# Kernel optimization log

Measured on AMD Instinct MI355X. Metric: run time of the kernel, lower is better.

## Reference

```python
import jax, jax.numpy as jnp
import numpy as np

B, S, D, H, HID = 4, 2048, 1024, 16, 4096
DK = D // H
EPS = 1e-6


def layernorm(x, alpha, bias):
    # Matches the custom LayerNorm: std with Bessel correction (torch default),
    # and eps added to std (not variance).
    mean = jnp.mean(x, axis=-1, keepdims=True)
    std = jnp.std(x, axis=-1, ddof=1, keepdims=True)
    return alpha * (x - mean) / (std + EPS) + bias


def setup_inputs() -> dict:
    key = jax.random.key(0)
    ks = jax.random.split(key, 10)
    s = 0.02
    return {
        "x": jax.random.normal(ks[0], (B, S, D), dtype=jnp.float32),
        "wq": jax.random.normal(ks[1], (D, D), dtype=jnp.float32) * s,
        "wk": jax.random.normal(ks[2], (D, D), dtype=jnp.float32) * s,
        "wv": jax.random.normal(ks[3], (D, D), dtype=jnp.float32) * s,
        "wo": jax.random.normal(ks[4], (D, D), dtype=jnp.float32) * s,
        "w1": jax.random.normal(ks[5], (D, HID), dtype=jnp.float32) * s,
        "b1": jnp.zeros((HID,), dtype=jnp.float32),
        "w2": jax.random.normal(ks[6], (HID, D), dtype=jnp.float32) * s,
        "b2": jnp.zeros((D,), dtype=jnp.float32),
        "ln1_a": jnp.ones((D,), dtype=jnp.float32),
        "ln1_b": jnp.zeros((D,), dtype=jnp.float32),
        "ln2_a": jnp.ones((D,), dtype=jnp.float32),
        "ln2_b": jnp.zeros((D,), dtype=jnp.float32),
    }


def reference(x, wq, wk, wv, wo, w1, b1, w2, b2, ln1_a, ln1_b, ln2_a, ln2_b):
    # --- residual 1: pre-norm self-attention ---
    h = layernorm(x, ln1_a, ln1_b)
    q = (h @ wq).reshape(B, S, H, DK)
    k = (h @ wk).reshape(B, S, H, DK)
    v = (h @ wv).reshape(B, S, H, DK)
    scores = jnp.einsum("bqhd,bkhd->bhqk", q, k) / jnp.sqrt(jnp.float32(DK))
    # Faithful replication of the original mask: tril on a (1, max_len) matrix
    # keeps only key position 0; all other key positions get -1e9.
    key_keep = (jnp.arange(S) == 0)  # [S]
    scores = jnp.where(key_keep[None, None, None, :], scores, jnp.float32(-1e9))
    attn = jax.nn.softmax(scores, axis=-1)  # [B,H,S,S]
    ctx = jnp.einsum("bhqk,bkhd->bqhd", attn, v).reshape(B, S, D)
    x = x + ctx @ wo
    # --- residual 2: pre-norm FFN ---
    h2 = layernorm(x, ln2_a, ln2_b)
    ff = jax.nn.gelu(h2 @ w1 + b1, approximate=False) @ w2 + b2
    return x + ff
```

## Files before the change

### kernel.cpp

```cpp
#include <hip/hip_runtime.h>
#include <cstdint>

#define D_MODEL 1024
#define HIDDEN  4096
#define BATCH   4
#define SEQ     2048
#define NROWS   (BATCH*SEQ)

typedef __attribute__((ext_vector_type(4))) int i32x4;

#define ACT_AMAX 4.0f
#define ACT_S    (ACT_AMAX / 127.0f)
#define ACT_INV  (127.0f / ACT_AMAX)

#define GLDS16(g, l) __builtin_amdgcn_global_load_lds(                        \
    (const __attribute__((address_space(1))) unsigned int*)(g),               \
    (__attribute__((address_space(3))) unsigned int*)(l), 16, 0, 0)

__device__ __forceinline__ float block_sum(float v, float* s4) {
  #pragma unroll
  for (int off = 32; off > 0; off >>= 1) v += __shfl_down(v, off);
  int lane = threadIdx.x & 63, wid = threadIdx.x >> 6;
  __syncthreads();
  if (lane == 0) s4[wid] = v;
  __syncthreads();
  return s4[0] + s4[1] + s4[2] + s4[3];
}

__device__ __forceinline__ float block_max(float v, float* s4) {
  #pragma unroll
  for (int off = 32; off > 0; off >>= 1) v = fmaxf(v, __shfl_down(v, off));
  int lane = threadIdx.x & 63, wid = threadIdx.x >> 6;
  __syncthreads();
  if (lane == 0) s4[wid] = v;
  __syncthreads();
  return fmaxf(fmaxf(s4[0], s4[1]), fmaxf(s4[2], s4[3]));
}

__device__ __forceinline__ signed char qclamp(float v) {
  float r = rintf(v);
  r = fminf(127.f, fmaxf(-127.f, r));
  return (signed char)(int)r;
}

#define KCHUNKS 32
#define KCH     (D_MODEL / KCHUNKS)


__device__ __forceinline__ void absmax_cols_body(
    const float* __restrict__ in, int R, int C, unsigned* __restrict__ u,
    int bx, int by) {
  int c  = bx * 256 + threadIdx.x;
  int r0 = by * 64;
  float m = 0.f;
  #pragma unroll 4
  for (int r = 0; r < 64; ++r)
    m = fmaxf(m, fabsf(in[(size_t)(r0 + r) * C + c]));
  atomicMax(&u[c], __float_as_uint(m));
}

__device__ __forceinline__ void transpose_quant_body(
    const float* __restrict__ in, signed char* __restrict__ out,
    int R, int C, const unsigned* __restrict__ u,
    float (*tile)[33], int bx, int by) {
  int c0 = bx * 32, r0 = by * 32;
  int tx = threadIdx.x & 31, ty = threadIdx.x >> 5;
  #pragma unroll
  for (int i = ty; i < 32; i += 8)
    tile[i][tx] = in[(size_t)(r0 + i) * C + c0 + tx];
  __syncthreads();
  #pragma unroll
  for (int i = ty; i < 32; i += 8) {
    float f = __uint_as_float(u[c0 + i]);
    float inv = f > 0.f ? 127.f / f : 0.f;
    out[(size_t)(c0 + i) * R + r0 + tx] = qclamp(tile[tx][i] * inv);
  }
}

__device__ __forceinline__ void ln_matvec_body(
    const float* __restrict__ x, const float* __restrict__ ln_a,
    const float* __restrict__ ln_b, const float* __restrict__ W,
    float* __restrict__ vout, float* s4, float (*hs)[KCH], int bx, int by) {
  int n  = bx * 256 + threadIdx.x;
  int k0 = by * KCH;
  int t  = threadIdx.x;
  float4 g4 = ((const float4*)ln_a)[t];
  float4 b4 = ((const float4*)ln_b)[t];
  #pragma unroll
  for (int b = 0; b < 4; ++b) {
    const float* xr = x + (size_t)b * SEQ * D_MODEL;
    float4 v = ((const float4*)xr)[t];
    float sum = v.x + v.y + v.z + v.w;
    float mean = block_sum(sum, s4) * (1.f / 1024.f);
    float cx = v.x - mean, cy = v.y - mean, cz = v.z - mean, cw = v.w - mean;
    float sq = cx * cx + cy * cy + cz * cz + cw * cw;
    float var = block_sum(sq, s4) * (1.f / 1023.f);
    float inv = 1.f / (sqrtf(var) + 1e-6f);
    if (t >= (k0 >> 2) && t < ((k0 + KCH) >> 2)) {
      int lc = 4 * t - k0;
      hs[b][lc + 0] = g4.x * cx * inv + b4.x;
      hs[b][lc + 1] = g4.y * cy * inv + b4.y;
      hs[b][lc + 2] = g4.z * cz * inv + b4.z;
      hs[b][lc + 3] = g4.w * cw * inv + b4.w;
    }
  }
  __syncthreads();
  float a0 = 0, a1 = 0, a2 = 0, a3 = 0;
  #pragma unroll
  for (int k = 0; k < KCH; ++k) {
    float w = W[(size_t)(k0 + k) * D_MODEL + n];
    a0 = fmaf(hs[0][k], w, a0);
    a1 = fmaf(hs[1][k], w, a1);
    a2 = fmaf(hs[2][k], w, a2);
    a3 = fmaf(hs[3][k], w, a3);
  }
  atomicAdd(&vout[0 * D_MODEL + n], a0);
  atomicAdd(&vout[1 * D_MODEL + n], a1);
  atomicAdd(&vout[2 * D_MODEL + n], a2);
  atomicAdd(&vout[3 * D_MODEL + n], a3);
}

__device__ __forceinline__ void matvec_body(
    const float* __restrict__ vin, const float* __restrict__ W,
    float* __restrict__ vout, float (*hs)[KCH], int bx, int by) {
  int n  = bx * 256 + threadIdx.x;
  int k0 = by * KCH;
  if (threadIdx.x < 4 * KCH)
    hs[threadIdx.x / KCH][threadIdx.x % KCH] =
        vin[(threadIdx.x / KCH) * D_MODEL + k0 + (threadIdx.x % KCH)];
  __syncthreads();
  float a0 = 0, a1 = 0, a2 = 0, a3 = 0;
  #pragma unroll
  for (int k = 0; k < KCH; ++k) {
    float w = W[(size_t)(k0 + k) * D_MODEL + n];
    a0 = fmaf(hs[0][k], w, a0);
    a1 = fmaf(hs[1][k], w, a1);
    a2 = fmaf(hs[2][k], w, a2);
    a3 = fmaf(hs[3][k], w, a3);
  }
  atomicAdd(&vout[0 * D_MODEL + n], a0);
  atomicAdd(&vout[1 * D_MODEL + n], a1);
  atomicAdd(&vout[2 * D_MODEL + n], a2);
  atomicAdd(&vout[3 * D_MODEL + n], a3);
}

__global__ __launch_bounds__(256) void pre1(
    const float* __restrict__ w1, const float* __restrict__ w2,
    unsigned* __restrict__ u1, unsigned* __restrict__ u2,
    const float* __restrict__ x, const float* __restrict__ ln1a,
    const float* __restrict__ ln1b, const float* __restrict__ wv,
    float* __restrict__ v0) {
  __shared__ float s4[4];
  __shared__ float hs[4][KCH];
  int id = blockIdx.x;
  if (id < 256) {
    absmax_cols_body(w1, D_MODEL, HIDDEN, u1, id & 15, id >> 4);
  } else if (id < 512) {
    int r = id - 256;
    absmax_cols_body(w2, HIDDEN, D_MODEL, u2, r & 3, r >> 2);
  } else {
    int r = id - 512;
    ln_matvec_body(x, ln1a, ln1b, wv, v0, s4, hs, r & 3, r >> 2);
  }
}

__global__ __launch_bounds__(256) void pre2(
    const float* __restrict__ w1, const float* __restrict__ w2,
    const unsigned* __restrict__ u1, const unsigned* __restrict__ u2,
    signed char* __restrict__ w1t, signed char* __restrict__ w2t,
    const float* __restrict__ v0, const float* __restrict__ wo,
    float* __restrict__ delta) {
  __shared__ float tile[32][33];
  __shared__ float hs[4][KCH];
  int id = blockIdx.x;
  if (id < 4096) {
    transpose_quant_body(w1, w1t, D_MODEL, HIDDEN, u1, tile, id & 127, id >> 7);
  } else if (id < 8192) {
    int r = id - 4096;
    transpose_quant_body(w2, w2t, HIDDEN, D_MODEL, u2, tile, r & 31, r >> 5);
  } else {
    int r = id - 8192;
    matvec_body(v0, wo, delta, hs, r & 3, r >> 2);
  }
}

__global__ __launch_bounds__(256) void fused_res_ln_q(
    const float* __restrict__ x, const float* __restrict__ delta,
    const float* __restrict__ g, const float* __restrict__ be,
    float* __restrict__ x1_out, signed char* __restrict__ h2,
    float* __restrict__ hscale) {
  __shared__ float s4[4];
  int row = blockIdx.x;
  int b = row >> 11;
  int t = threadIdx.x;
  float4 v  = ((const float4*)(x + (size_t)row * D_MODEL))[t];
  float4 d4 = ((const float4*)(delta + (size_t)b * D_MODEL))[t];
  v.x += d4.x; v.y += d4.y; v.z += d4.z; v.w += d4.w;
  float sum = v.x + v.y + v.z + v.w;
  float mean = block_sum(sum, s4) * (1.f / 1024.f);
  float cx = v.x - mean, cy = v.y - mean, cz = v.z - mean, cw = v.w - mean;
  float sq = cx * cx + cy * cy + cz * cz + cw * cw;
  float var = block_sum(sq, s4) * (1.f / 1023.f);
  float inv = 1.f / (sqrtf(var) + 1e-6f);
  ((float4*)(x1_out + (size_t)row * D_MODEL))[t] = v;
  float4 g4 = ((const float4*)g)[t];
  float4 b4 = ((const float4*)be)[t];
  float h0v = g4.x * cx * inv + b4.x;
  float h1v = g4.y * cy * inv + b4.y;
  float h2v = g4.z * cz * inv + b4.z;
  float h3v = g4.w * cw * inv + b4.w;
  float am = fmaxf(fmaxf(fabsf(h0v), fabsf(h1v)), fmaxf(fabsf(h2v), fabsf(h3v)));
  float amax = block_max(am, s4);
  float qs = amax > 0.f ? 127.f / amax : 0.f;
  unsigned q = ((unsigned)(unsigned char)(int)qclamp(h0v * qs)) |
               ((unsigned)(unsigned char)(int)qclamp(h1v * qs) << 8) |
               ((unsigned)(unsigned char)(int)qclamp(h2v * qs) << 16) |
               ((unsigned)(unsigned char)(int)qclamp(h3v * qs) << 24);
  ((unsigned*)(h2 + (size_t)row * D_MODEL))[t] = q;
  if (t == 0) hscale[row] = amax * (1.f / 127.f);
}

template <int EPI>
__global__ __launch_bounds__(256, 3) void gemm_i8(
    const signed char* __restrict__ A, const signed char* __restrict__ Bt,
    const float* __restrict__ rowS, float rowConst,
    const unsigned* __restrict__ colU, const float* __restrict__ bias,
    signed char* __restrict__ Cq, float* __restrict__ Cf, int M, int N, int K) {
  __shared__ signed char LA[128][128];
  __shared__ signed char LB[128][128];

  int GN  = N / 128;
  int nwg = (M / 128) * GN;
  int id  = blockIdx.x;
  int sw  = (id & 7) * (nwg >> 3) + (id >> 3);
  int by  = sw / GN, bx = sw % GN;
  int m0  = by * 128, n0 = bx * 128;
  int NT  = K / 128;

  int t = threadIdx.x;
  int wid = t >> 6, lane = t & 63;
  int wm = wid >> 1, wn = wid & 1;
  int lr = lane & 15, kg = lane >> 4;
  int swz = (lr & 7) << 4;

  int rS = t >> 3;
  int cS = ((t & 7) ^ (rS & 7)) * 16;
  const signed char* Ag = A  + (size_t)(m0 + rS) * K + cS;
  const signed char* Bg = Bt + (size_t)(n0 + rS) * K + cS;
  int ldsOff = wid * 1024;

#define STG_T(T) do {                                                          \
    size_t ko_ = (size_t)(T) * 128;                                            \
    GLDS16(Ag + ko_,                  &LA[0][0] + ldsOff);                     \
    GLDS16(Ag + ko_ + (size_t)32 * K, &LA[0][0] + ldsOff + 4096);              \
    GLDS16(Ag + ko_ + (size_t)64 * K, &LA[0][0] + ldsOff + 8192);              \
    GLDS16(Ag + ko_ + (size_t)96 * K, &LA[0][0] + ldsOff + 12288);             \
    GLDS16(Bg + ko_,                  &LB[0][0] + ldsOff);                     \
    GLDS16(Bg + ko_ + (size_t)32 * K, &LB[0][0] + ldsOff + 4096);              \
    GLDS16(Bg + ko_ + (size_t)64 * K, &LB[0][0] + ldsOff + 8192);              \
    GLDS16(Bg + ko_ + (size_t)96 * K, &LB[0][0] + ldsOff + 12288);             \
  } while (0)

#define RD_AB() do {                                                           \
    _Pragma("unroll") for (int mi = 0; mi < 4; ++mi)                           \
    _Pragma("unroll") for (int kk = 0; kk < 2; ++kk)                           \
      a[mi][kk] = *(const i32x4*)                                              \
          &LA[wm * 64 + mi * 16 + lr][(kk * 64 + kg * 16) ^ swz];              \
    _Pragma("unroll") for (int ni = 0; ni < 4; ++ni)                           \
    _Pragma("unroll") for (int kk = 0; kk < 2; ++kk)                           \
      b[ni][kk] = *(const i32x4*)                                              \
          &LB[wn * 64 + ni * 16 + lr][(kk * 64 + kg * 16) ^ swz];              \
  } while (0)

#define MM_ALL() do {                                                          \
    _Pragma("unroll") for (int mi = 0; mi < 4; ++mi)                           \
    _Pragma("unroll") for (int ni = 0; ni < 4; ++ni)                           \
    _Pragma("unroll") for (int kk = 0; kk < 2; ++kk)                           \
      acc[mi][ni] = __builtin_amdgcn_mfma_i32_16x16x64_i8(                     \
          a[mi][kk], b[ni][kk], acc[mi][ni], 0, 0, 0);                         \
  } while (0)

  i32x4 acc[4][4] = {};
  i32x4 a[4][2];
  i32x4 b[4][2];

  for (int tt = 0; tt < NT; ++tt) {
    STG_T(tt);
    asm volatile("s_waitcnt vmcnt(0)" ::: "memory");
    __builtin_amdgcn_s_barrier();
    RD_AB();
    MM_ALL();
    __builtin_amdgcn_s_barrier();
  }

  int orow = m0 + wm * 64;
  int ocol = n0 + wn * 64;
  #pragma unroll
  for (int mf = 0; mf < 4; ++mf) {
    #pragma unroll
    for (int nf = 0; nf < 4; ++nf) {
      int col = ocol + nf * 16 + lr;
      float cs = __uint_as_float(colU[col]) * (1.f / 127.f);
      float bz = bias[col];
      #pragma unroll
      for (int j = 0; j < 4; ++j) {
        int row = orow + mf * 16 + kg * 4 + j;
        float rs = (EPI == 0) ? rowS[row] : rowConst;
        float val = (float)acc[mf][nf][j] * rs * cs + bz;
        if (EPI == 0) {
          float u = val * (0.7978845608f + 0.0356774081f * val * val);
          float e = __expf(2.f * u);
          float th = 1.f - 2.f / (e + 1.f);
          val = 0.5f * val * (1.f + th);
          Cq[(size_t)row * N + col] = qclamp(val * ACT_INV);
        } else {
          size_t idx = (size_t)row * N + col;
          Cf[idx] = Cf[idx] + val;
        }
      }
    }
  }
#undef STG_T
#undef RD_AB
#undef MM_ALL
}

__global__ __launch_bounds__(256, 3) void gemm2_sk2(
    const signed char* __restrict__ A, const signed char* __restrict__ Bt,
    const unsigned* __restrict__ colU, const float* __restrict__ bias,
    float* __restrict__ Cf) {
  constexpr int M = NROWS, N = D_MODEL, K = HIDDEN;
  constexpr int GN = N / 128;
  constexpr int PS = (M / 128) * GN;
  constexpr int NT = (K / 2) / 128;

  __shared__ signed char LA[128][128];
  __shared__ signed char LB[128][128];

  int id = blockIdx.x;
  int sw = (id & 7) * 128 + (id >> 3);
  int ks = sw >> 9;
  int rem = sw & (PS - 1);
  int by = rem >> 3, bx = rem & (GN - 1);
  int m0 = by * 128, n0 = bx * 128;
  int k0s = ks * (K / 2);

  int t = threadIdx.x;
  int wid = t >> 6, lane = t & 63;
  int wm = wid >> 1, wn = wid & 1;
  int lr = lane & 15, kg = lane >> 4;
  int swz = (lr & 7) << 4;

  int rS = t >> 3;
  int cS = ((t & 7) ^ (rS & 7)) * 16;
  const signed char* Ag = A  + (size_t)(m0 + rS) * K + k0s + cS;
  const signed char* Bg = Bt + (size_t)(n0 + rS) * K + k0s + cS;
  int ldsOff = wid * 1024;

#define STG_T(T) do {                                                          \
    size_t ko_ = (size_t)(T) * 128;                                            \
    GLDS16(Ag + ko_,                  &LA[0][0] + ldsOff);                     \
    GLDS16(Ag + ko_ + (size_t)32 * K, &LA[0][0] + ldsOff + 4096);              \
    GLDS16(Ag + ko_ + (size_t)64 * K, &LA[0][0] + ldsOff + 8192);              \
    GLDS16(Ag + ko_ + (size_t)96 * K, &LA[0][0] + ldsOff + 12288);             \
    GLDS16(Bg + ko_,                  &LB[0][0] + ldsOff);                     \
    GLDS16(Bg + ko_ + (size_t)32 * K, &LB[0][0] + ldsOff + 4096);              \
    GLDS16(Bg + ko_ + (size_t)64 * K, &LB[0][0] + ldsOff + 8192);              \
    GLDS16(Bg + ko_ + (size_t)96 * K, &LB[0][0] + ldsOff + 12288);             \
  } while (0)

#define RD_AB() do {                                                           \
    _Pragma("unroll") for (int mi = 0; mi < 4; ++mi)                           \
    _Pragma("unroll") for (int kk = 0; kk < 2; ++kk)                           \
      a[mi][kk] = *(const i32x4*)                                              \
          &LA[wm * 64 + mi * 16 + lr][(kk * 64 + kg * 16) ^ swz];              \
    _Pragma("unroll") for (int ni = 0; ni < 4; ++ni)                           \
    _Pragma("unroll") for (int kk = 0; kk < 2; ++kk)                           \
      b[ni][kk] = *(const i32x4*)                                              \
          &LB[wn * 64 + ni * 16 + lr][(kk * 64 + kg * 16) ^ swz];              \
  } while (0)

#define MM_ALL() do {                                                          \
    _Pragma("unroll") for (int mi = 0; mi < 4; ++mi)                           \
    _Pragma("unroll") for (int ni = 0; ni < 4; ++ni)                           \
    _Pragma("unroll") for (int kk = 0; kk < 2; ++kk)                           \
      acc[mi][ni] = __builtin_amdgcn_mfma_i32_16x16x64_i8(                     \
          a[mi][kk], b[ni][kk], acc[mi][ni], 0, 0, 0);                         \
  } while (0)

  i32x4 acc[4][4] = {};
  i32x4 a[4][2];
  i32x4 b[4][2];

  for (int tt = 0; tt < NT; ++tt) {
    STG_T(tt);
    asm volatile("s_waitcnt vmcnt(0)" ::: "memory");
    __builtin_amdgcn_s_barrier();
    RD_AB();
    MM_ALL();
    __builtin_amdgcn_s_barrier();
  }

  int orow = m0 + wm * 64;
  int ocol = n0 + wn * 64;
  #pragma unroll
  for (int mf = 0; mf < 4; ++mf) {
    #pragma unroll
    for (int nf = 0; nf < 4; ++nf) {
      int col = ocol + nf * 16 + lr;
      float cs = __uint_as_float(colU[col]) * (1.f / 127.f);
      float bz = (ks == 0) ? bias[col] : 0.f;
      #pragma unroll
      for (int j = 0; j < 4; ++j) {
        int row = orow + mf * 16 + kg * 4 + j;
        float val = (float)acc[mf][nf][j] * ACT_S * cs + bz;
        atomicAdd(&Cf[(size_t)row * N + col], val);
      }
    }
  }
#undef STG_T
#undef RD_AB
#undef MM_ALL
}

extern "C" void kernel_launch(void* const* d_in, const int* in_sizes, int n_in,
                              void* d_out, int out_size, void* d_ws, size_t ws_size,
                              hipStream_t stream) {
  const float* x    = (const float*)d_in[0];
  const float* wv   = (const float*)d_in[3];
  const float* wo   = (const float*)d_in[4];
  const float* w1   = (const float*)d_in[5];
  const float* b1   = (const float*)d_in[6];
  const float* w2   = (const float*)d_in[7];
  const float* b2   = (const float*)d_in[8];
  const float* ln1a = (const float*)d_in[9];
  const float* ln1b = (const float*)d_in[10];
  const float* ln2a = (const float*)d_in[11];
  const float* ln2b = (const float*)d_in[12];
  float* out = (float*)d_out;

  char* ws = (char*)d_ws;
  signed char* w1t = (signed char*)(ws);
  signed char* w2t = (signed char*)(ws + (4ull  << 20));
  signed char* h2  = (signed char*)(ws + (8ull  << 20));
  signed char* act = (signed char*)(ws + (16ull << 20));
  char* sc = ws + (48ull << 20);
  unsigned* u1    = (unsigned*)(sc);
  unsigned* u2    = (unsigned*)(sc + 16384);
  float*    v0    = (float*)(sc + 20480);
  float*    delta = (float*)(sc + 36864);
  float*    hsc   = (float*)(sc + 53248);

  hipMemsetAsync(sc, 0, 53248, stream);

  pre1<<<640, 256, 0, stream>>>(w1, w2, u1, u2, x, ln1a, ln1b, wv, v0);

  pre2<<<8320, 256, 0, stream>>>(w1, w2, u1, u2, w1t, w2t, v0, wo, delta);

  fused_res_ln_q<<<NROWS, 256, 0, stream>>>(x, delta, ln2a, ln2b, out, h2, hsc);

  gemm_i8<0><<<(NROWS / 128) * (HIDDEN / 128), 256, 0, stream>>>(
      h2, w1t, hsc, 0.f, u1, b1, act, nullptr, NROWS, HIDDEN, D_MODEL);

  gemm2_sk2<<<1024, 256, 0, stream>>>(act, w2t, u2, b2, out);
}
```

Before: 197.0 us.

## Replace split-K atomic GEMM2 with K=256 tile kernel and XCD-aware block mapping

The second FFN GEMM drops its 2-way split-K with atomicAdd epilogue and becomes a templated kernel that stages 256-wide K slices per iteration (double the LDS per block, occupancy hint lowered to 2) and does a plain read-add-write into the output. Both GEMMs also replace the strided block swizzle with a mapping that gives each XCD a contiguous 2D region of output tiles, aiming for better L2 reuse per die. The intent is to remove atomic traffic and halve barrier and loop overhead per K. The cost is 512 blocks instead of 1024 for GEMM2, less parallelism and lower occupancy.

```diff
diff --git a/kernel.cpp b/kernel.cpp
--- a/kernel.cpp
+++ b/kernel.cpp
@@ -221,7 +221,7 @@
 }
 
 template <int EPI>
-__global__ __launch_bounds__(256, 3) void gemm_i8(
+__global__ __launch_bounds__(256, 3) void gemm_k128(
     const signed char* __restrict__ A, const signed char* __restrict__ Bt,
     const float* __restrict__ rowS, float rowConst,
     const unsigned* __restrict__ colU, const float* __restrict__ bias,
@@ -230,10 +230,14 @@
   __shared__ signed char LB[128][128];
 
   int GN  = N / 128;
-  int nwg = (M / 128) * GN;
+  int CX  = (GN >= 16) ? 16 : (GN >> 1);
   int id  = blockIdx.x;
-  int sw  = (id & 7) * (nwg >> 3) + (id >> 3);
-  int by  = sw / GN, bx = sw % GN;
+  int xcd = id & 7;
+  int r   = id >> 3;
+  int cby = xcd >> 1, cbx = xcd & 1;
+  int lby = r / CX,   lbx = r % CX;
+  int by  = cby * 16 + lby;
+  int bx  = cbx * CX + lbx;
   int m0  = by * 128, n0 = bx * 128;
   int NT  = K / 128;
 
@@ -325,25 +329,26 @@
 #undef MM_ALL
 }
 
-__global__ __launch_bounds__(256, 3) void gemm2_sk2(
+template <int EPI>
+__global__ __launch_bounds__(256, 2) void gemm_k256(
     const signed char* __restrict__ A, const signed char* __restrict__ Bt,
+    const float* __restrict__ rowS, float rowConst,
     const unsigned* __restrict__ colU, const float* __restrict__ bias,
-    float* __restrict__ Cf) {
-  constexpr int M = NROWS, N = D_MODEL, K = HIDDEN;
-  constexpr int GN = N / 128;
-  constexpr int PS = (M / 128) * GN;
-  constexpr int NT = (K / 2) / 128;
-
-  __shared__ signed char LA[128][128];
-  __shared__ signed char LB[128][128];
-
-  int id = blockIdx.x;
-  int sw = (id & 7) * 128 + (id >> 3);
-  int ks = sw >> 9;
-  int rem = sw & (PS - 1);
-  int by = rem >> 3, bx = rem & (GN - 1);
-  int m0 = by * 128, n0 = bx * 128;
-  int k0s = ks * (K / 2);
+    signed char* __restrict__ Cq, float* __restrict__ Cf, int M, int N, int K) {
+  __shared__ signed char LA[128][256];
+  __shared__ signed char LB[128][256];
+
+  int GN  = N / 128;
+  int CX  = (GN >= 16) ? 16 : (GN >> 1);
+  int id  = blockIdx.x;
+  int xcd = id & 7;
+  int r   = id >> 3;
+  int cby = xcd >> 1, cbx = xcd & 1;
+  int lby = r / CX,   lbx = r % CX;
+  int by  = cby * 16 + lby;
+  int bx  = cbx * CX + lbx;
+  int m0  = by * 128, n0 = bx * 128;
+  int NT  = K / 256;
 
   int t = threadIdx.x;
   int wid = t >> 6, lane = t & 63;
@@ -351,31 +356,29 @@
   int lr = lane & 15, kg = lane >> 4;
   int swz = (lr & 7) << 4;
 
-  int rS = t >> 3;
-  int cS = ((t & 7) ^ (rS & 7)) * 16;
-  const signed char* Ag = A  + (size_t)(m0 + rS) * K + k0s + cS;
-  const signed char* Bg = Bt + (size_t)(n0 + rS) * K + k0s + cS;
+  int rS = t >> 4;
+  int cS = ((t & 15) ^ (rS & 7)) * 16;
+  const signed char* Ag = A  + (size_t)(m0 + rS) * K + cS;
+  const signed char* Bg = Bt + (size_t)(n0 + rS) * K + cS;
   int ldsOff = wid * 1024;
 
 #define STG_T(T) do {                                                          \
-    size_t ko_ = (size_t)(T) * 128;                                            \
-    GLDS16(Ag + ko_,                  &LA[0][0] + ldsOff);                     \
-    GLDS16(Ag + ko_ + (size_t)32 * K, &LA[0][0] + ldsOff + 4096);              \
-    GLDS16(Ag + ko_ + (size_t)64 * K, &LA[0][0] + ldsOff + 8192);              \
-    GLDS16(Ag + ko_ + (size_t)96 * K, &LA[0][0] + ldsOff + 12288);             \
-    GLDS16(Bg + ko_,                  &LB[0][0] + ldsOff);                     \
-    GLDS16(Bg + ko_ + (size_t)32 * K, &LB[0][0] + ldsOff + 4096);              \
-    GLDS16(Bg + ko_ + (size_t)64 * K, &LB[0][0] + ldsOff + 8192);              \
-    GLDS16(Bg + ko_ + (size_t)96 * K, &LB[0][0] + ldsOff + 12288);             \
+    size_t ko_ = (size_t)(T) * 256;                                            \
+    _Pragma("unroll") for (int j = 0; j < 8; ++j)                              \
+      GLDS16(Ag + ko_ + (size_t)(16 * j) * K,                                  \
+             &LA[0][0] + ldsOff + j * 4096);                                   \
+    _Pragma("unroll") for (int j = 0; j < 8; ++j)                              \
+      GLDS16(Bg + ko_ + (size_t)(16 * j) * K,                                  \
+             &LB[0][0] + ldsOff + j * 4096);                                   \
   } while (0)
 
 #define RD_AB() do {                                                           \
     _Pragma("unroll") for (int mi = 0; mi < 4; ++mi)                           \
-    _Pragma("unroll") for (int kk = 0; kk < 2; ++kk)                           \
+    _Pragma("unroll") for (int kk = 0; kk < 4; ++kk)                           \
       a[mi][kk] = *(const i32x4*)                                              \
           &LA[wm * 64 + mi * 16 + lr][(kk * 64 + kg * 16) ^ swz];              \
     _Pragma("unroll") for (int ni = 0; ni < 4; ++ni)                           \
-    _Pragma("unroll") for (int kk = 0; kk < 2; ++kk)                           \
+    _Pragma("unroll") for (int kk = 0; kk < 4; ++kk)                           \
       b[ni][kk] = *(const i32x4*)                                              \
           &LB[wn * 64 + ni * 16 + lr][(kk * 64 + kg * 16) ^ swz];              \
   } while (0)
@@ -383,14 +386,14 @@
 #define MM_ALL() do {                                                          \
     _Pragma("unroll") for (int mi = 0; mi < 4; ++mi)                           \
     _Pragma("unroll") for (int ni = 0; ni < 4; ++ni)                           \
-    _Pragma("unroll") for (int kk = 0; kk < 2; ++kk)                           \
+    _Pragma("unroll") for (int kk = 0; kk < 4; ++kk)                           \
       acc[mi][ni] = __builtin_amdgcn_mfma_i32_16x16x64_i8(                     \
           a[mi][kk], b[ni][kk], acc[mi][ni], 0, 0, 0);                         \
   } while (0)
 
   i32x4 acc[4][4] = {};
-  i32x4 a[4][2];
-  i32x4 b[4][2];
+  i32x4 a[4][4];
+  i32x4 b[4][4];
 
   for (int tt = 0; tt < NT; ++tt) {
     STG_T(tt);
@@ -409,12 +412,22 @@
     for (int nf = 0; nf < 4; ++nf) {
       int col = ocol + nf * 16 + lr;
       float cs = __uint_as_float(colU[col]) * (1.f / 127.f);
-      float bz = (ks == 0) ? bias[col] : 0.f;
+      float bz = bias[col];
       #pragma unroll
       for (int j = 0; j < 4; ++j) {
         int row = orow + mf * 16 + kg * 4 + j;
-        float val = (float)acc[mf][nf][j] * ACT_S * cs + bz;
-        atomicAdd(&Cf[(size_t)row * N + col], val);
+        float rs = (EPI == 0) ? rowS[row] : rowConst;
+        float val = (float)acc[mf][nf][j] * rs * cs + bz;
+        if (EPI == 0) {
+          float u = val * (0.7978845608f + 0.0356774081f * val * val);
+          float e = __expf(2.f * u);
+          float th = 1.f - 2.f / (e + 1.f);
+          val = 0.5f * val * (1.f + th);
+          Cq[(size_t)row * N + col] = qclamp(val * ACT_INV);
+        } else {
+          size_t idx = (size_t)row * N + col;
+          Cf[idx] = Cf[idx] + val;
+        }
       }
     }
   }
@@ -459,8 +472,9 @@
 
   fused_res_ln_q<<<NROWS, 256, 0, stream>>>(x, delta, ln2a, ln2b, out, h2, hsc);
 
-  gemm_i8<0><<<(NROWS / 128) * (HIDDEN / 128), 256, 0, stream>>>(
+  gemm_k128<0><<<(NROWS / 128) * (HIDDEN / 128), 256, 0, stream>>>(
       h2, w1t, hsc, 0.f, u1, b1, act, nullptr, NROWS, HIDDEN, D_MODEL);
 
-  gemm2_sk2<<<1024, 256, 0, stream>>>(act, w2t, u2, b2, out);
-}
+  gemm_k256<1><<<(NROWS / 128) * (D_MODEL / 128), 256, 0, stream>>>(
+      act, w2t, nullptr, ACT_S, u2, b2, nullptr, out, NROWS, D_MODEL, HIDDEN);
+}
```

Measured after the change: 167.0 us. -15.2%, faster.
